# Kernel optimization log

Measured on AMD Instinct MI355X. Metric: run time of the kernel, lower is better.

## Reference

```python
import jax, jax.numpy as jnp
import numpy as np

N = 8192   # nodes
F = 16     # node features (col 0 = signal, last 3 = xyz)
H = 64     # hidden
G = 256    # number of graphs (segments)
EPS = 1e-3 # keras LayerNormalization default epsilon


def setup_inputs() -> dict:
    key = jax.random.key(0)
    ks = jax.random.split(key, 10)
    s = 0.05
    X = jax.random.normal(ks[0], (N, F), jnp.float32)
    # dense pre-normalized adjacency (spektral GCNConv expects normalized A)
    A = jax.random.uniform(ks[1], (N, N), jnp.float32) * (1.0 / N)
    I = jnp.sort(jax.random.randint(ks[2], (N,), 0, G)).astype(jnp.int32)
    W0 = jax.random.normal(ks[3], (F, H), jnp.float32) * s
    b0 = jnp.zeros((H,), jnp.float32)
    g0 = jnp.ones((H,), jnp.float32)
    be0 = jnp.zeros((H,), jnp.float32)
    W1 = jax.random.normal(ks[4], (H, H), jnp.float32) * s
    b1 = jnp.zeros((H,), jnp.float32)
    g1 = jnp.ones((H,), jnp.float32)
    be1 = jnp.zeros((H,), jnp.float32)
    Wf = jax.random.normal(ks[5], (H, H), jnp.float32) * s
    bf = jnp.zeros((H,), jnp.float32)
    Wa = jax.random.normal(ks[6], (H, H), jnp.float32) * s
    ba = jnp.zeros((H,), jnp.float32)
    Wout = jax.random.normal(ks[7], (H + 3, 3), jnp.float32) * s
    bout = jnp.zeros((3,), jnp.float32)
    return dict(X=X, A=A, I=I, W0=W0, b0=b0, g0=g0, be0=be0,
                W1=W1, b1=b1, g1=g1, be1=be1,
                Wf=Wf, bf=bf, Wa=Wa, ba=ba, Wout=Wout, bout=bout)


def _layer_norm(x, gamma, beta):
    m = jnp.mean(x, axis=-1, keepdims=True)
    v = jnp.mean(jnp.square(x - m), axis=-1, keepdims=True)
    return (x - m) * jax.lax.rsqrt(v + EPS) * gamma + beta


def reference(X, A, I, W0, b0, g0, be0, W1, b1, g1, be1, Wf, bf, Wa, ba, Wout, bout):
    I = I.astype(jnp.int32)
    # GCN layer 0: relu(A @ X @ W0 + b0) -> LayerNorm
    h0 = _layer_norm(jax.nn.relu(A @ (X @ W0) + b0), g0, be0)
    # GCN layer 1 + LayerNorm + residual (i > 0)
    h = _layer_norm(jax.nn.relu(A @ (h0 @ W1) + b1), g1, be1) + h0
    # GlobalAttentionPool: Dense features * sigmoid-gated attention, segment-summed per graph
    feat = h @ Wf + bf                       # [N, H]
    attn = jax.nn.sigmoid(h @ Wa + ba)       # [N, H]
    g = jax.ops.segment_sum(feat * attn, I, num_segments=G)  # [G, H]
    # Signal-weighted barycentre via segment-softmax over log1p(relu(signal))
    z = jnp.log1p(jax.nn.relu(X[:, 0]))                       # [N]
    zmax = jax.ops.segment_max(z, I, num_segments=G)          # [G]
    zexp = jnp.exp(z - zmax[I])                               # [N]
    zsum = jax.ops.segment_sum(zexp, I, num_segments=G)       # [G]
    w = zexp / zsum[I]                                        # [N]
    bary = jax.ops.segment_sum(w[:, None] * X[:, -3:], I, num_segments=G)  # [G, 3]
    return jnp.concatenate([g, bary], axis=-1) @ Wout + bout  # [G, 3]
```

## Files before the change

### kernel.cpp

```cpp
#include <hip/hip_runtime.h>
#include <hip/hip_bf16.h>
#include <math.h>

#define NN 8192
#define FF 16
#define HH 64
#define GG 256
#define LN_EPS 1e-3f
#define KSPLIT 8
#define KC (NN / KSPLIT)

typedef __bf16 bf16x8 __attribute__((ext_vector_type(8)));
typedef float  floatx4 __attribute__((ext_vector_type(4)));

__global__ void k1_xw0(const float* __restrict__ X,
                       const float* __restrict__ W0,
                       const int* __restrict__ I,
                       __hip_bfloat16* __restrict__ Zt0,
                       float* __restrict__ zarr,
                       unsigned int* __restrict__ zmax_bits) {
    const int b = blockIdx.x, tid = threadIdx.x;
    const int lane = tid & 63;
    const int i = (b & 127) * 64 + lane;
    const int n = ((b >> 7) << 2) + (tid >> 6);
    float s = 0.f;
#pragma unroll
    for (int m = 0; m < FF; ++m)
        s += X[i * FF + m] * W0[m * HH + n];
    Zt0[(size_t)n * NN + i] = __float2bfloat16(s);

    if (b < 128 && tid < 64) {
        const int ii = b * 64 + lane;
        float z = log1pf(fmaxf(X[ii * FF], 0.f));
        zarr[ii] = z;
        atomicMax(&zmax_bits[I[ii]], __float_as_uint(z));
    }
}

__global__ __launch_bounds__(256)
void k_gemm_split(const float* __restrict__ A,
                  const __hip_bfloat16* __restrict__ Zt,
                  float* __restrict__ C) {
    const int tid  = threadIdx.x;
    const int wave = tid >> 6;
    const int lane = tid & 63;
    const int l16  = lane & 15;
    const int quad = lane >> 4;
    const int rb   = blockIdx.x & 127;
    const int kb   = blockIdx.x >> 7;
    const int row0 = rb * 64;
    const int k0   = kb * KC;

    const float* aptr = A + (size_t)(row0 + wave * 16 + l16) * NN + k0 + quad * 8;
    const __hip_bfloat16* bp0 = Zt + (size_t)(0 * 16 + l16) * NN + k0 + quad * 8;
    const __hip_bfloat16* bp1 = Zt + (size_t)(1 * 16 + l16) * NN + k0 + quad * 8;
    const __hip_bfloat16* bp2 = Zt + (size_t)(2 * 16 + l16) * NN + k0 + quad * 8;
    const __hip_bfloat16* bp3 = Zt + (size_t)(3 * 16 + l16) * NN + k0 + quad * 8;

    floatx4 acc0 = {0.f,0.f,0.f,0.f}, acc1 = {0.f,0.f,0.f,0.f};
    floatx4 acc2 = {0.f,0.f,0.f,0.f}, acc3 = {0.f,0.f,0.f,0.f};

#pragma unroll 4
    for (int k = 0; k < KC; k += 32) {
        const float4 a0 = *reinterpret_cast<const float4*>(aptr + k);
        const float4 a1 = *reinterpret_cast<const float4*>(aptr + k + 4);
        bf16x8 af;
        af[0] = (__bf16)a0.x; af[1] = (__bf16)a0.y;
        af[2] = (__bf16)a0.z; af[3] = (__bf16)a0.w;
        af[4] = (__bf16)a1.x; af[5] = (__bf16)a1.y;
        af[6] = (__bf16)a1.z; af[7] = (__bf16)a1.w;
        const bf16x8 b0 = *reinterpret_cast<const bf16x8*>(bp0 + k);
        const bf16x8 b1 = *reinterpret_cast<const bf16x8*>(bp1 + k);
        const bf16x8 b2 = *reinterpret_cast<const bf16x8*>(bp2 + k);
        const bf16x8 b3 = *reinterpret_cast<const bf16x8*>(bp3 + k);
        acc0 = __builtin_amdgcn_mfma_f32_16x16x32_bf16(af, b0, acc0, 0, 0, 0);
        acc1 = __builtin_amdgcn_mfma_f32_16x16x32_bf16(af, b1, acc1, 0, 0, 0);
        acc2 = __builtin_amdgcn_mfma_f32_16x16x32_bf16(af, b2, acc2, 0, 0, 0);
        acc3 = __builtin_amdgcn_mfma_f32_16x16x32_bf16(af, b3, acc3, 0, 0, 0);
    }

    const size_t rbase = (size_t)(row0 + wave * 16 + quad * 4);
#pragma unroll
    for (int r = 0; r < 4; ++r) {
        float* crow = C + (rbase + r) * HH + l16;
        atomicAdd(crow +  0, acc0[r]);
        atomicAdd(crow + 16, acc1[r]);
        atomicAdd(crow + 32, acc2[r]);
        atomicAdd(crow + 48, acc3[r]);
    }
}

__global__ __launch_bounds__(256)
void k_ln(const float* __restrict__ C,
          const float* __restrict__ bias,
          const float* __restrict__ gamma,
          const float* __restrict__ beta,
          const float* __restrict__ resid,
          float* __restrict__ out) {
    const int tid = threadIdx.x;
    const int row = tid >> 4;
    const int c0  = (tid & 15) * 4;
    const size_t grow = (size_t)(blockIdx.x * 16 + row);

    float4 v4 = *reinterpret_cast<const float4*>(&C[grow * HH + c0]);
    const float4 b4 = *reinterpret_cast<const float4*>(&bias[c0]);
    float v[4] = { fmaxf(v4.x + b4.x, 0.f), fmaxf(v4.y + b4.y, 0.f),
                   fmaxf(v4.z + b4.z, 0.f), fmaxf(v4.w + b4.w, 0.f) };
    float s = 0.f, ss = 0.f;
#pragma unroll
    for (int j = 0; j < 4; ++j) { s += v[j]; ss += v[j] * v[j]; }
#pragma unroll
    for (int m = 1; m < 16; m <<= 1) {
        s  += __shfl_xor(s,  m, 64);
        ss += __shfl_xor(ss, m, 64);
    }
    const float mean = s * (1.f / 64.f);
    const float var  = fmaxf(ss * (1.f / 64.f) - mean * mean, 0.f);
    const float inv  = rsqrtf(var + LN_EPS);
    const float4 g4  = *reinterpret_cast<const float4*>(&gamma[c0]);
    const float4 be4 = *reinterpret_cast<const float4*>(&beta[c0]);
    float4 o;
    o.x = (v[0] - mean) * inv * g4.x + be4.x;
    o.y = (v[1] - mean) * inv * g4.y + be4.y;
    o.z = (v[2] - mean) * inv * g4.z + be4.z;
    o.w = (v[3] - mean) * inv * g4.w + be4.w;
    if (resid) {
        const float4 r4 = *reinterpret_cast<const float4*>(&resid[grow * HH + c0]);
        o.x += r4.x; o.y += r4.y; o.z += r4.z; o.w += r4.w;
    }
    *reinterpret_cast<float4*>(&out[grow * HH + c0]) = o;
}

__global__ void k3_hw1(const float* __restrict__ h0,
                       const float* __restrict__ W1,
                       __hip_bfloat16* __restrict__ Zt1) {
    const int b = blockIdx.x, tid = threadIdx.x;
    const int lane = tid & 63;
    const int i = (b & 127) * 64 + lane;
    const int n = ((b >> 7) << 2) + (tid >> 6);
    float s = 0.f;
#pragma unroll 8
    for (int m = 0; m < HH; ++m)
        s += h0[(size_t)i * HH + m] * W1[m * HH + n];
    Zt1[(size_t)n * NN + i] = __float2bfloat16(s);
}

__global__ __launch_bounds__(256)
void k5_pool(const float* __restrict__ h,
             const float* __restrict__ Wf, const float* __restrict__ bfv,
             const float* __restrict__ Wa, const float* __restrict__ bav,
             const int* __restrict__ I,
             float* __restrict__ g) {
    __shared__ float hrow[4][64];
    const int w = threadIdx.x >> 6, l = threadIdx.x & 63;
    const int node = blockIdx.x * 4 + w;
    hrow[w][l] = h[(size_t)node * HH + l];
    __syncthreads();
    float sf = bfv[l], sa = bav[l];
#pragma unroll 8
    for (int m = 0; m < HH; ++m) {
        const float hv = hrow[w][m];
        sf += hv * Wf[m * HH + l];
        sa += hv * Wa[m * HH + l];
    }
    const float attn = 1.f / (1.f + expf(-sa));
    atomicAdd(&g[(size_t)I[node] * HH + l], sf * attn);
}

__global__ void k6_bary(const float* __restrict__ X,
                        const int* __restrict__ I,
                        const float* __restrict__ zarr,
                        const float* __restrict__ zmax,
                        float* __restrict__ zsum,
                        float* __restrict__ baryn) {
    const int i = blockIdx.x * 256 + threadIdx.x;
    const int seg = I[i];
    const float ze = expf(zarr[i] - zmax[seg]);
    atomicAdd(&zsum[seg], ze);
    atomicAdd(&baryn[seg * 3 + 0], ze * X[i * FF + 13]);
    atomicAdd(&baryn[seg * 3 + 1], ze * X[i * FF + 14]);
    atomicAdd(&baryn[seg * 3 + 2], ze * X[i * FF + 15]);
}

__global__ void k7_out(const float* __restrict__ g,
                       const float* __restrict__ zsum,
                       const float* __restrict__ baryn,
                       const float* __restrict__ Wout,
                       const float* __restrict__ bout,
                       float* __restrict__ out) {
    const int w = threadIdx.x >> 6, lane = threadIdx.x & 63;
    const int gi = blockIdx.x * 4 + w;
    const float vg = g[(size_t)gi * HH + lane];
    const float zs = zsum[gi];
    const float invz = (zs > 0.f) ? (1.f / zs) : 0.f;
    const float extra = (lane < 3) ? baryn[gi * 3 + lane] * invz : 0.f;
#pragma unroll
    for (int d = 0; d < 3; ++d) {
        float p = vg * Wout[lane * 3 + d];
        if (lane < 3) p += extra * Wout[(64 + lane) * 3 + d];
#pragma unroll
        for (int m = 1; m < 64; m <<= 1) p += __shfl_xor(p, m, 64);
        if (lane == 0) out[gi * 3 + d] = p + bout[d];
    }
}

extern "C" void kernel_launch(void* const* d_in, const int* in_sizes, int n_in,
                              void* d_out, int out_size, void* d_ws, size_t ws_size,
                              hipStream_t stream) {
    const float* X   = (const float*)d_in[0];
    const float* A   = (const float*)d_in[1];
    const int*   I   = (const int*)d_in[2];
    const float* W0  = (const float*)d_in[3];
    const float* b0  = (const float*)d_in[4];
    const float* g0  = (const float*)d_in[5];
    const float* be0 = (const float*)d_in[6];
    const float* W1  = (const float*)d_in[7];
    const float* b1  = (const float*)d_in[8];
    const float* g1  = (const float*)d_in[9];
    const float* be1 = (const float*)d_in[10];
    const float* Wf  = (const float*)d_in[11];
    const float* bfv = (const float*)d_in[12];
    const float* Wa  = (const float*)d_in[13];
    const float* bav = (const float*)d_in[14];
    const float* Wo  = (const float*)d_in[15];
    const float* bo  = (const float*)d_in[16];

    char* ws = (char*)d_ws;
    float* C0   = (float*)(ws);
    float* C1   = (float*)(ws + (2u << 20));
    float* accr = (float*)(ws + (4u << 20));
    float* g     = accr;
    float* zmax  = accr + GG * HH;
    float* zsum  = zmax + GG;
    float* baryn = zsum + GG;
    const size_t memset_bytes = (size_t)(2 * NN * HH + GG * HH + GG + GG + GG * 3) * sizeof(float);

    __hip_bfloat16* Zt0 = (__hip_bfloat16*)(ws + (4u << 20) + (128u << 10));
    __hip_bfloat16* Zt1 = (__hip_bfloat16*)(ws + (5u << 20) + (128u << 10));
    float* h0   = (float*)(ws + (6u << 20) + (128u << 10));
    float* h    = (float*)(ws + (8u << 20) + (128u << 10));
    float* zarr = (float*)(ws + (10u << 20) + (128u << 10));

    hipMemsetAsync(ws, 0, memset_bytes, stream);

    k1_xw0<<<2048, 256, 0, stream>>>(X, W0, I, Zt0, zarr, (unsigned int*)zmax);
    k_gemm_split<<<1024, 256, 0, stream>>>(A, Zt0, C0);
    k_ln<<<512, 256, 0, stream>>>(C0, b0, g0, be0, nullptr, h0);
    k3_hw1<<<2048, 256, 0, stream>>>(h0, W1, Zt1);
    k_gemm_split<<<1024, 256, 0, stream>>>(A, Zt1, C1);
    k_ln<<<512, 256, 0, stream>>>(C1, b1, g1, be1, h0, h);
    k5_pool<<<2048, 256, 0, stream>>>(h, Wf, bfv, Wa, bav, I, g);
    k6_bary<<<32, 256, 0, stream>>>(X, I, zarr, zmax, zsum, baryn);
    k7_out<<<64, 256, 0, stream>>>(g, zsum, baryn, Wo, bo, (float*)d_out);
}
```

Baseline: 602.0 us.

## Fuse pipeline into cooperative persistent kernel with split-K partial buffers

Replaces the nine separate launches and the memset with one cooperative kernel whose phases are separated by grid-wide syncs, with a multi-kernel fallback. Split-K GEMM results are now written to per-split partial buffers and summed inside the LayerNorm phase instead of using float atomics. H@W1 is fused into the first LayerNorm phase using shared-memory tiles, and the barycentre accumulation is folded into the pooling phase. The cost is grid-sync overhead, more partial-buffer traffic, and a dependence on occupancy allowing 1024 co-resident blocks.

Measured after the change: 618.9 us. 1.03x slower.

```diff
diff --git a/kernel.cpp b/kernel.cpp
--- a/kernel.cpp
+++ b/kernel.cpp
@@ -1,6 +1,9 @@
 #include <hip/hip_runtime.h>
 #include <hip/hip_bf16.h>
+#include <hip/hip_cooperative_groups.h>
 #include <math.h>
+
+namespace cg = cooperative_groups;
 
 #define NN 8192
 #define FF 16
@@ -9,45 +12,75 @@
 #define LN_EPS 1e-3f
 #define KSPLIT 8
 #define KC (NN / KSPLIT)
+#define NBLK 1024
+
+#define OFF_G     0
+#define OFF_ZMAX  (GG * HH)
+#define OFF_ZSUM  (GG * HH + GG)
+#define OFF_BARY  (GG * HH + 2 * GG)
+#define ACC_TOT   (GG * HH + 2 * GG + 3 * GG)
 
 typedef __bf16 bf16x8 __attribute__((ext_vector_type(8)));
 typedef float  floatx4 __attribute__((ext_vector_type(4)));
 
-__global__ void k1_xw0(const float* __restrict__ X,
-                       const float* __restrict__ W0,
-                       const int* __restrict__ I,
-                       __hip_bfloat16* __restrict__ Zt0,
-                       float* __restrict__ zarr,
-                       unsigned int* __restrict__ zmax_bits) {
-    const int b = blockIdx.x, tid = threadIdx.x;
-    const int lane = tid & 63;
-    const int i = (b & 127) * 64 + lane;
-    const int n = ((b >> 7) << 2) + (tid >> 6);
-    float s = 0.f;
-#pragma unroll
-    for (int m = 0; m < FF; ++m)
-        s += X[i * FF + m] * W0[m * HH + n];
-    Zt0[(size_t)n * NN + i] = __float2bfloat16(s);
-
-    if (b < 128 && tid < 64) {
-        const int ii = b * 64 + lane;
-        float z = log1pf(fmaxf(X[ii * FF], 0.f));
-        zarr[ii] = z;
-        atomicMax(&zmax_bits[I[ii]], __float_as_uint(z));
-    }
-}
-
-__global__ __launch_bounds__(256)
-void k_gemm_split(const float* __restrict__ A,
-                  const __hip_bfloat16* __restrict__ Zt,
-                  float* __restrict__ C) {
-    const int tid  = threadIdx.x;
+struct Args {
+    const float* X; const float* A; const int* I;
+    const float* W0; const float* b0; const float* g0; const float* be0;
+    const float* W1; const float* b1; const float* g1; const float* be1;
+    const float* Wf; const float* bf; const float* Wa; const float* ba;
+    const float* Wo; const float* bo;
+    float* Cp; __hip_bfloat16* Zt0; __hip_bfloat16* Zt1;
+    float* h0; float* h; float* zarr; float* acc; float* out;
+};
+
+union SM {
+    struct { float Xs[64][17]; } p0;
+    struct { float hs[16][65]; float Ws[64][65]; } p2;
+};
+
+__device__ __forceinline__ void phase_zero(const Args& a, int bid, int t) {
+    const int idx = bid * 256 + t;
+    if (idx < ACC_TOT) a.acc[idx] = 0.f;
+}
+
+__device__ __forceinline__ void phase0(const Args& a, SM& sm, int bid, int t) {
+    const int tile = bid >> 3, cgp = bid & 7;
+    const int i0 = tile * 64;
+    {
+        const int r = t >> 2, c = (t & 3) * 4;
+        const float4 v = *reinterpret_cast<const float4*>(&a.X[(size_t)(i0 + r) * FF + c]);
+        sm.p0.Xs[r][c + 0] = v.x; sm.p0.Xs[r][c + 1] = v.y;
+        sm.p0.Xs[r][c + 2] = v.z; sm.p0.Xs[r][c + 3] = v.w;
+    }
+    __syncthreads();
+    const int i = t & 63;
+    const int n = cgp * 8 + ((t >> 6) << 1);
+    float s0 = 0.f, s1 = 0.f;
+#pragma unroll
+    for (int m = 0; m < FF; ++m) {
+        const float hv = sm.p0.Xs[i][m];
+        const float2 w = *reinterpret_cast<const float2*>(&a.W0[m * HH + n]);
+        s0 += hv * w.x; s1 += hv * w.y;
+    }
+    a.Zt0[(size_t)n * NN + i0 + i]       = __float2bfloat16(s0);
+    a.Zt0[(size_t)(n + 1) * NN + i0 + i] = __float2bfloat16(s1);
+    if (cgp == 0 && t < 64) {
+        const float z = log1pf(fmaxf(sm.p0.Xs[t][0], 0.f));
+        a.zarr[i0 + t] = z;
+        atomicMax(reinterpret_cast<unsigned int*>(a.acc + OFF_ZMAX) + a.I[i0 + t],
+                  __float_as_uint(z));
+    }
+}
+
+__device__ __forceinline__ void phase_gemm(const float* __restrict__ A,
+                                           const __hip_bfloat16* __restrict__ Zt,
+                                           float* __restrict__ Cp, int bid, int tid) {
     const int wave = tid >> 6;
     const int lane = tid & 63;
     const int l16  = lane & 15;
     const int quad = lane >> 4;
-    const int rb   = blockIdx.x & 127;
-    const int kb   = blockIdx.x >> 7;
+    const int rb   = bid & 127;
+    const int kb   = bid >> 7;
     const int row0 = rb * 64;
     const int k0   = kb * KC;
 
@@ -79,33 +112,29 @@
         acc3 = __builtin_amdgcn_mfma_f32_16x16x32_bf16(af, b3, acc3, 0, 0, 0);
     }
 
-    const size_t rbase = (size_t)(row0 + wave * 16 + quad * 4);
+    float* cp = Cp + ((size_t)kb * NN + row0 + wave * 16 + quad * 4) * HH + l16;
 #pragma unroll
     for (int r = 0; r < 4; ++r) {
-        float* crow = C + (rbase + r) * HH + l16;
-        atomicAdd(crow +  0, acc0[r]);
-        atomicAdd(crow + 16, acc1[r]);
-        atomicAdd(crow + 32, acc2[r]);
-        atomicAdd(crow + 48, acc3[r]);
-    }
-}
-
-__global__ __launch_bounds__(256)
-void k_ln(const float* __restrict__ C,
-          const float* __restrict__ bias,
-          const float* __restrict__ gamma,
-          const float* __restrict__ beta,
-          const float* __restrict__ resid,
-          float* __restrict__ out) {
-    const int tid = threadIdx.x;
-    const int row = tid >> 4;
-    const int c0  = (tid & 15) * 4;
-    const size_t grow = (size_t)(blockIdx.x * 16 + row);
-
-    float4 v4 = *reinterpret_cast<const float4*>(&C[grow * HH + c0]);
+        cp[(size_t)r * HH +  0] = acc0[r];
+        cp[(size_t)r * HH + 16] = acc1[r];
+        cp[(size_t)r * HH + 32] = acc2[r];
+        cp[(size_t)r * HH + 48] = acc3[r];
+    }
+}
+
+__device__ __forceinline__ float4 ln_core(const Args& a, const float* bias,
+                                          const float* gamma, const float* beta,
+                                          size_t grow, int c0) {
+    float4 acc4 = {0.f, 0.f, 0.f, 0.f};
+#pragma unroll
+    for (int kb = 0; kb < KSPLIT; ++kb) {
+        const float4 v = *reinterpret_cast<const float4*>(
+            &a.Cp[((size_t)kb * NN + grow) * HH + c0]);
+        acc4.x += v.x; acc4.y += v.y; acc4.z += v.z; acc4.w += v.w;
+    }
     const float4 b4 = *reinterpret_cast<const float4*>(&bias[c0]);
-    float v[4] = { fmaxf(v4.x + b4.x, 0.f), fmaxf(v4.y + b4.y, 0.f),
-                   fmaxf(v4.z + b4.z, 0.f), fmaxf(v4.w + b4.w, 0.f) };
+    float v[4] = { fmaxf(acc4.x + b4.x, 0.f), fmaxf(acc4.y + b4.y, 0.f),
+                   fmaxf(acc4.z + b4.z, 0.f), fmaxf(acc4.w + b4.w, 0.f) };
     float s = 0.f, ss = 0.f;
 #pragma unroll
     for (int j = 0; j < 4; ++j) { s += v[j]; ss += v[j] * v[j]; }
@@ -124,132 +153,179 @@
     o.y = (v[1] - mean) * inv * g4.y + be4.y;
     o.z = (v[2] - mean) * inv * g4.z + be4.z;
     o.w = (v[3] - mean) * inv * g4.w + be4.w;
-    if (resid) {
-        const float4 r4 = *reinterpret_cast<const float4*>(&resid[grow * HH + c0]);
-        o.x += r4.x; o.y += r4.y; o.z += r4.z; o.w += r4.w;
-    }
-    *reinterpret_cast<float4*>(&out[grow * HH + c0]) = o;
-}
-
-__global__ void k3_hw1(const float* __restrict__ h0,
-                       const float* __restrict__ W1,
-                       __hip_bfloat16* __restrict__ Zt1) {
-    const int b = blockIdx.x, tid = threadIdx.x;
-    const int lane = tid & 63;
-    const int i = (b & 127) * 64 + lane;
-    const int n = ((b >> 7) << 2) + (tid >> 6);
-    float s = 0.f;
-#pragma unroll 8
-    for (int m = 0; m < HH; ++m)
-        s += h0[(size_t)i * HH + m] * W1[m * HH + n];
-    Zt1[(size_t)n * NN + i] = __float2bfloat16(s);
-}
-
-__global__ __launch_bounds__(256)
-void k5_pool(const float* __restrict__ h,
-             const float* __restrict__ Wf, const float* __restrict__ bfv,
-             const float* __restrict__ Wa, const float* __restrict__ bav,
-             const int* __restrict__ I,
-             float* __restrict__ g) {
-    __shared__ float hrow[4][64];
-    const int w = threadIdx.x >> 6, l = threadIdx.x & 63;
-    const int node = blockIdx.x * 4 + w;
-    hrow[w][l] = h[(size_t)node * HH + l];
+    return o;
+}
+
+__device__ __forceinline__ void phase2(const Args& a, SM& sm, int bid, int t) {
+    if (bid >= 512) return;
+    const int row = t >> 4, c0 = (t & 15) * 4;
+    const size_t grow0 = (size_t)bid * 16;
+    const size_t grow  = grow0 + row;
+    const float4 o = ln_core(a, a.b0, a.g0, a.be0, grow, c0);
+    *reinterpret_cast<float4*>(&a.h0[grow * HH + c0]) = o;
+    sm.p2.hs[row][c0 + 0] = o.x; sm.p2.hs[row][c0 + 1] = o.y;
+    sm.p2.hs[row][c0 + 2] = o.z; sm.p2.hs[row][c0 + 3] = o.w;
+#pragma unroll
+    for (int p = 0; p < 4; ++p) {
+        const int idx = p * 256 + t;
+        const int r = idx >> 4, c = (idx & 15) * 4;
+        const float4 w = *reinterpret_cast<const float4*>(&a.W1[(size_t)r * HH + c]);
+        sm.p2.Ws[r][c + 0] = w.x; sm.p2.Ws[r][c + 1] = w.y;
+        sm.p2.Ws[r][c + 2] = w.z; sm.p2.Ws[r][c + 3] = w.w;
+    }
     __syncthreads();
-    float sf = bfv[l], sa = bav[l];
+    const int n = t & 63, rq = t >> 6;
+    float s0 = 0.f, s1 = 0.f, s2 = 0.f, s3 = 0.f;
 #pragma unroll 8
     for (int m = 0; m < HH; ++m) {
-        const float hv = hrow[w][m];
-        sf += hv * Wf[m * HH + l];
-        sa += hv * Wa[m * HH + l];
-    }
-    const float attn = 1.f / (1.f + expf(-sa));
-    atomicAdd(&g[(size_t)I[node] * HH + l], sf * attn);
-}
-
-__global__ void k6_bary(const float* __restrict__ X,
-                        const int* __restrict__ I,
-                        const float* __restrict__ zarr,
-                        const float* __restrict__ zmax,
-                        float* __restrict__ zsum,
-                        float* __restrict__ baryn) {
-    const int i = blockIdx.x * 256 + threadIdx.x;
-    const int seg = I[i];
-    const float ze = expf(zarr[i] - zmax[seg]);
-    atomicAdd(&zsum[seg], ze);
-    atomicAdd(&baryn[seg * 3 + 0], ze * X[i * FF + 13]);
-    atomicAdd(&baryn[seg * 3 + 1], ze * X[i * FF + 14]);
-    atomicAdd(&baryn[seg * 3 + 2], ze * X[i * FF + 15]);
-}
-
-__global__ void k7_out(const float* __restrict__ g,
-                       const float* __restrict__ zsum,
-                       const float* __restrict__ baryn,
-                       const float* __restrict__ Wout,
-                       const float* __restrict__ bout,
-                       float* __restrict__ out) {
-    const int w = threadIdx.x >> 6, lane = threadIdx.x & 63;
-    const int gi = blockIdx.x * 4 + w;
-    const float vg = g[(size_t)gi * HH + lane];
-    const float zs = zsum[gi];
+        const float w = sm.p2.Ws[m][n];
+        s0 += sm.p2.hs[rq * 4 + 0][m] * w;
+        s1 += sm.p2.hs[rq * 4 + 1][m] * w;
+        s2 += sm.p2.hs[rq * 4 + 2][m] * w;
+        s3 += sm.p2.hs[rq * 4 + 3][m] * w;
+    }
+    __hip_bfloat16 hb0 = __float2bfloat16(s0), hb1 = __float2bfloat16(s1);
+    __hip_bfloat16 hb2 = __float2bfloat16(s2), hb3 = __float2bfloat16(s3);
+    ushort4 u;
+    u.x = *reinterpret_cast<unsigned short*>(&hb0);
+    u.y = *reinterpret_cast<unsigned short*>(&hb1);
+    u.z = *reinterpret_cast<unsigned short*>(&hb2);
+    u.w = *reinterpret_cast<unsigned short*>(&hb3);
+    *reinterpret_cast<ushort4*>(&a.Zt1[(size_t)n * NN + grow0 + rq * 4]) = u;
+}
+
+__device__ __forceinline__ void phase4(const Args& a, int bid, int t) {
+    if (bid >= 512) return;
+    const int row = t >> 4, c0 = (t & 15) * 4;
+    const size_t grow = (size_t)bid * 16 + row;
+    float4 o = ln_core(a, a.b1, a.g1, a.be1, grow, c0);
+    const float4 r4 = *reinterpret_cast<const float4*>(&a.h0[grow * HH + c0]);
+    o.x += r4.x; o.y += r4.y; o.z += r4.z; o.w += r4.w;
+    *reinterpret_cast<float4*>(&a.h[grow * HH + c0]) = o;
+}
+
+__device__ __forceinline__ void phase5(const Args& a, int bid, int t) {
+    const int w = t >> 6, l = t & 63;
+#pragma unroll
+    for (int rep = 0; rep < 2; ++rep) {
+        const int node = rep * 4096 + bid * 4 + w;
+        const float hvl = a.h[(size_t)node * HH + l];
+        float sf = a.bf[l], sa = a.ba[l];
+#pragma unroll 8
+        for (int m = 0; m < HH; ++m) {
+            const float hv = __shfl(hvl, m, 64);
+            sf += hv * a.Wf[m * HH + l];
+            sa += hv * a.Wa[m * HH + l];
+        }
+        const float attn = 1.f / (1.f + expf(-sa));
+        const int seg = a.I[node];
+        atomicAdd(&a.acc[OFF_G + (size_t)seg * HH + l], sf * attn);
+        if (l < 4) {
+            const float ze = expf(a.zarr[node] - a.acc[OFF_ZMAX + seg]);
+            if (l == 0) atomicAdd(&a.acc[OFF_ZSUM + seg], ze);
+            else        atomicAdd(&a.acc[OFF_BARY + seg * 3 + (l - 1)],
+                                  ze * a.X[(size_t)node * FF + 12 + l]);
+        }
+    }
+}
+
+__device__ __forceinline__ void phase6(const Args& a, int bid, int t) {
+    if (bid >= 64) return;
+    const int w = t >> 6, lane = t & 63;
+    const int gi = bid * 4 + w;
+    const float vg = a.acc[OFF_G + (size_t)gi * HH + lane];
+    const float zs = a.acc[OFF_ZSUM + gi];
     const float invz = (zs > 0.f) ? (1.f / zs) : 0.f;
-    const float extra = (lane < 3) ? baryn[gi * 3 + lane] * invz : 0.f;
+    const float extra = (lane < 3) ? a.acc[OFF_BARY + gi * 3 + lane] * invz : 0.f;
 #pragma unroll
     for (int d = 0; d < 3; ++d) {
-        float p = vg * Wout[lane * 3 + d];
-        if (lane < 3) p += extra * Wout[(64 + lane) * 3 + d];
+        float p = vg * a.Wo[lane * 3 + d];
+        if (lane < 3) p += extra * a.Wo[(HH + lane) * 3 + d];
 #pragma unroll
         for (int m = 1; m < 64; m <<= 1) p += __shfl_xor(p, m, 64);
-        if (lane == 0) out[gi * 3 + d] = p + bout[d];
-    }
-}
+        if (lane == 0) a.out[gi * 3 + d] = p + a.bo[d];
+    }
+}
+
+__global__ __launch_bounds__(256, 4) void mega(Args a) {
+    __shared__ SM sm;
+    cg::grid_group grid = cg::this_grid();
+    const int bid = blockIdx.x, t = threadIdx.x;
+    phase_zero(a, bid, t);                 grid.sync();
+    phase0(a, sm, bid, t);                 grid.sync();
+    phase_gemm(a.A, a.Zt0, a.Cp, bid, t);  grid.sync();
+    phase2(a, sm, bid, t);                 grid.sync();
+    phase_gemm(a.A, a.Zt1, a.Cp, bid, t);  grid.sync();
+    phase4(a, bid, t);                     grid.sync();
+    phase5(a, bid, t);                     grid.sync();
+    phase6(a, bid, t);
+}
+
+__global__ __launch_bounds__(256, 4) void k_pz(Args a){ phase_zero(a, blockIdx.x, threadIdx.x); }
+__global__ __launch_bounds__(256, 4) void k_p0(Args a){ __shared__ SM sm; phase0(a, sm, blockIdx.x, threadIdx.x); }
+__global__ __launch_bounds__(256, 4) void k_pg0(Args a){ phase_gemm(a.A, a.Zt0, a.Cp, blockIdx.x, threadIdx.x); }
+__global__ __launch_bounds__(256, 4) void k_p2(Args a){ __shared__ SM sm; phase2(a, sm, blockIdx.x, threadIdx.x); }
+__global__ __launch_bounds__(256, 4) void k_pg1(Args a){ phase_gemm(a.A, a.Zt1, a.Cp, blockIdx.x, threadIdx.x); }
+__global__ __launch_bounds__(256, 4) void k_p4(Args a){ phase4(a, blockIdx.x, threadIdx.x); }
+__global__ __launch_bounds__(256, 4) void k_p5(Args a){ phase5(a, blockIdx.x, threadIdx.x); }
+__global__ __launch_bounds__(256, 4) void k_p6(Args a){ phase6(a, blockIdx.x, threadIdx.x); }
 
 extern "C" void kernel_launch(void* const* d_in, const int* in_sizes, int n_in,
                               void* d_out, int out_size, void* d_ws, size_t ws_size,
                               hipStream_t stream) {
-    const float* X   = (const float*)d_in[0];
-    const float* A   = (const float*)d_in[1];
-    const int*   I   = (const int*)d_in[2];
-    const float* W0  = (const float*)d_in[3];
-    const float* b0  = (const float*)d_in[4];
-    const float* g0  = (const float*)d_in[5];
-    const float* be0 = (const float*)d_in[6];
-    const float* W1  = (const float*)d_in[7];
-    const float* b1  = (const float*)d_in[8];
-    const float* g1  = (const float*)d_in[9];
-    const float* be1 = (const float*)d_in[10];
-    const float* Wf  = (const float*)d_in[11];
-    const float* bfv = (const float*)d_in[12];
-    const float* Wa  = (const float*)d_in[13];
-    const float* bav = (const float*)d_in[14];
-    const float* Wo  = (const float*)d_in[15];
-    const float* bo  = (const float*)d_in[16];
+    Args a;
+    a.X   = (const float*)d_in[0];
+    a.A   = (const float*)d_in[1];
+    a.I   = (const int*)d_in[2];
+    a.W0  = (const float*)d_in[3];
+    a.b0  = (const float*)d_in[4];
+    a.g0  = (const float*)d_in[5];
+    a.be0 = (const float*)d_in[6];
+    a.W1  = (const float*)d_in[7];
+    a.b1  = (const float*)d_in[8];
+    a.g1  = (const float*)d_in[9];
+    a.be1 = (const float*)d_in[10];
+    a.Wf  = (const float*)d_in[11];
+    a.bf  = (const float*)d_in[12];
+    a.Wa  = (const float*)d_in[13];
+    a.ba  = (const float*)d_in[14];
+    a.Wo  = (const float*)d_in[15];
+    a.bo  = (const float*)d_in[16];
 
     char* ws = (char*)d_ws;
-    float* C0   = (float*)(ws);
-    float* C1   = (float*)(ws + (2u << 20));
-    float* accr = (float*)(ws + (4u << 20));
-    float* g     = accr;
-    float* zmax  = accr + GG * HH;
-    float* zsum  = zmax + GG;
-    float* baryn = zsum + GG;
-    const size_t memset_bytes = (size_t)(2 * NN * HH + GG * HH + GG + GG + GG * 3) * sizeof(float);
-
-    __hip_bfloat16* Zt0 = (__hip_bfloat16*)(ws + (4u << 20) + (128u << 10));
-    __hip_bfloat16* Zt1 = (__hip_bfloat16*)(ws + (5u << 20) + (128u << 10));
-    float* h0   = (float*)(ws + (6u << 20) + (128u << 10));
-    float* h    = (float*)(ws + (8u << 20) + (128u << 10));
-    float* zarr = (float*)(ws + (10u << 20) + (128u << 10));
-
-    hipMemsetAsync(ws, 0, memset_bytes, stream);
-
-    k1_xw0<<<2048, 256, 0, stream>>>(X, W0, I, Zt0, zarr, (unsigned int*)zmax);
-    k_gemm_split<<<1024, 256, 0, stream>>>(A, Zt0, C0);
-    k_ln<<<512, 256, 0, stream>>>(C0, b0, g0, be0, nullptr, h0);
-    k3_hw1<<<2048, 256, 0, stream>>>(h0, W1, Zt1);
-    k_gemm_split<<<1024, 256, 0, stream>>>(A, Zt1, C1);
-    k_ln<<<512, 256, 0, stream>>>(C1, b1, g1, be1, h0, h);
-    k5_pool<<<2048, 256, 0, stream>>>(h, Wf, bfv, Wa, bav, I, g);
-    k6_bary<<<32, 256, 0, stream>>>(X, I, zarr, zmax, zsum, baryn);
-    k7_out<<<64, 256, 0, stream>>>(g, zsum, baryn, Wo, bo, (float*)d_out);
-}
+    a.Cp   = (float*)ws;
+    a.Zt0  = (__hip_bfloat16*)(ws + (16u << 20));
+    a.Zt1  = (__hip_bfloat16*)(ws + (17u << 20));
+    a.h0   = (float*)(ws + (18u << 20));
+    a.h    = (float*)(ws + (20u << 20));
+    a.zarr = (float*)(ws + (22u << 20));
+    a.acc  = (float*)(ws + (22u << 20) + (64u << 10));
+    a.out  = (float*)d_out;
+
+    static int coop = -1;
+    if (coop < 0) {
+        int occ = 0, ncu = 0, dev = 0;
+        hipGetDevice(&dev);
+        hipOccupancyMaxActiveBlocksPerMultiprocessor(&occ, mega, 256, 0);
+        hipDeviceGetAttribute(&ncu, hipDeviceAttributeMultiprocessorCount, dev);
+        coop = (occ * ncu >= NBLK) ? 1 : 0;
+    }
+
+    bool launched = false;
+    if (coop) {
+        void* kargs[] = { (void*)&a };
+        hipError_t err = hipLaunchCooperativeKernel(
+            reinterpret_cast<const void*>(mega), dim3(NBLK), dim3(256), kargs, 0, stream);
+        launched = (err == hipSuccess);
+    }
+    if (!launched) {
+        k_pz <<<NBLK, 256, 0, stream>>>(a);
+        k_p0 <<<NBLK, 256, 0, stream>>>(a);
+        k_pg0<<<NBLK, 256, 0, stream>>>(a);
+        k_p2 <<<512,  256, 0, stream>>>(a);
+        k_pg1<<<NBLK, 256, 0, stream>>>(a);
+        k_p4 <<<512,  256, 0, stream>>>(a);
+        k_p5 <<<NBLK, 256, 0, stream>>>(a);
+        k_p6 <<<64,   256, 0, stream>>>(a);
+    }
+}
```
